# Kernel tuning notes

Hardware: AMD Instinct MI355X
Metric: run time of the kernel (lower is better)

Reference implementation:

```python
import jax, jax.numpy as jnp
import numpy as np

EPS = 1e-5

def _bn(z, g, b):
    # train-mode BatchNorm2d: batch stats over (B,H,W), biased variance
    mean = z.mean(axis=(0, 2, 3), keepdims=True)
    var = z.var(axis=(0, 2, 3), keepdims=True)
    return g[None, :, None, None] * (z - mean) * jax.lax.rsqrt(var + EPS) + b[None, :, None, None]

def _conv1x1(x, w):
    # x: [B,C,H,W], w: [O,C] -> [B,O,H,W]
    return jnp.einsum('bchw,oc->bohw', x, w)

def _proj(x, w1, g1, b1, w2, g2, b2):
    z = _bn(_conv1x1(x, w1), g1, b1)
    return _bn(_conv1x1(z, w2), g2, b2)

def setup_inputs() -> dict:
    key = jax.random.key(0)
    ks = jax.random.split(key, 24)
    B, Cx, Cy, M, H, W = 4, 512, 256, 64, 64, 64
    f32 = jnp.float32
    def wmat(k, o, c):
        return jax.random.normal(k, (o, c), f32) * (c ** -0.5)
    def gamma(k, c):
        return 1.0 + 0.1 * jax.random.normal(k, (c,), f32)
    def beta(k, c):
        return 0.1 * jax.random.normal(k, (c,), f32)
    inp = {
        'x': jax.random.normal(ks[0], (B, Cx, H, W), f32),
        'y': jax.random.normal(ks[1], (B, Cy, H, W), f32),
        # f_self
        'ws1': wmat(ks[2], M, Cx), 'gs1': gamma(ks[3], M), 'bs1': beta(ks[4], M),
        'ws2': wmat(ks[5], M, M),  'gs2': gamma(ks[6], M), 'bs2': beta(ks[7], M),
        # f_x
        'wx1': wmat(ks[8], M, Cx), 'gx1': gamma(ks[9], M), 'bx1': beta(ks[10], M),
        'wx2': wmat(ks[11], M, M), 'gx2': gamma(ks[12], M), 'bx2': beta(ks[13], M),
        # f_y
        'wy1': wmat(ks[14], M, Cy), 'gy1': gamma(ks[15], M), 'by1': beta(ks[16], M),
        'wy2': wmat(ks[17], M, M),  'gy2': gamma(ks[18], M), 'by2': beta(ks[19], M),
        # f_up
        'wu': wmat(ks[20], Cx, M), 'gu': gamma(ks[21], Cx), 'bu': beta(ks[22], Cx),
    }
    return inp

def reference(x, y, ws1, gs1, bs1, ws2, gs2, bs2,
              wx1, gx1, bx1, wx2, gx2, bx2,
              wy1, gy1, by1, wy2, gy2, by2,
              wu, gu, bu):
    B, C, H, W = x.shape
    M = ws1.shape[0]
    N = H * W
    fself = _proj(x, ws1, gs1, bs1, ws2, gs2, bs2).reshape(B, M, N).transpose(0, 2, 1)  # [B,N,M]
    fx = _proj(x, wx1, gx1, bx1, wx2, gx2, bx2).reshape(B, M, N).transpose(0, 2, 1)      # [B,N,M]
    fy = _proj(y, wy1, gy1, by1, wy2, gy2, by2).reshape(B, M, N)                          # [B,M,N]
    sim = jnp.matmul(fx, fy)                  # [B,N,N]  (scale=False)
    attn = jax.nn.softmax(sim, axis=-1)
    fout = jnp.matmul(attn, fself)            # [B,N,M]
    fout = fout.transpose(0, 2, 1).reshape(B, M, H, W)
    out = _bn(_conv1x1(fout, wu), gu, bu)
    return x + out
```

## Files before the change

### kernel.cpp

```cpp
#include <hip/hip_runtime.h>
#include <hip/hip_fp16.h>
#include <cstdint>

constexpr int N_ = 4096;
constexpr float CNT = 16384.f;

typedef __attribute__((ext_vector_type(8))) _Float16 half8;
typedef __attribute__((ext_vector_type(4))) float f32x4;
union fragh { half8 h8; int i4[4]; };

__device__ inline int pkh(float a, float b) {
  union { __half2 h; int i; } u;
  u.h = __float22half2_rn(float2{a, b});
  return u.i;
}


__global__ __launch_bounds__(256) void conv1_k(
    const float* __restrict__ x, const float* __restrict__ y,
    const float* __restrict__ ws1, const float* __restrict__ wx1,
    const float* __restrict__ wy1,
    float* __restrict__ z1s, float* __restrict__ z1x, float* __restrict__ z1y,
    float* __restrict__ stats) {
  const int t = threadIdx.x;
  const int slice = blockIdx.x;
  const int b = slice >> 5;
  const int n0 = (slice & 31) * 128;
  const int branch = blockIdx.y;
  const float* A = branch == 2 ? y : x;
  const float* W = branch == 0 ? ws1 : (branch == 1 ? wx1 : wy1);
  float* out = branch == 0 ? z1s : (branch == 1 ? z1x : z1y);
  const int K = branch == 2 ? 256 : 512;
  float* st = stats + branch * 128;

  __shared__ float sA[32][132];
  __shared__ float sW[32][72];

  const int to = (t >> 5) * 8;
  const int tn = (t & 31) * 4;
  float acc[8][4];
#pragma unroll
  for (int i = 0; i < 8; ++i)
#pragma unroll
    for (int j = 0; j < 4; ++j) acc[i][j] = 0.f;

  const float* Ab = A + (size_t)b * K * N_ + n0;
#pragma unroll 1
  for (int k0 = 0; k0 < K; k0 += 32) {
    __syncthreads();
#pragma unroll
    for (int i = 0; i < 4; ++i) {
      int row = i * 8 + (t >> 5);
      float4 v = *(const float4*)&Ab[(size_t)(k0 + row) * N_ + tn];
      *(float4*)&sA[row][tn] = v;
    }
    {
      int o = t >> 2, kk = (t & 3) * 8;
      float4 w0 = *(const float4*)&W[(size_t)o * K + k0 + kk];
      float4 w1 = *(const float4*)&W[(size_t)o * K + k0 + kk + 4];
      sW[kk + 0][o] = w0.x; sW[kk + 1][o] = w0.y;
      sW[kk + 2][o] = w0.z; sW[kk + 3][o] = w0.w;
      sW[kk + 4][o] = w1.x; sW[kk + 5][o] = w1.y;
      sW[kk + 6][o] = w1.z; sW[kk + 7][o] = w1.w;
    }
    __syncthreads();
#pragma unroll
    for (int k = 0; k < 32; ++k) {
      float4 a = *(const float4*)&sA[k][tn];
      float4 w0 = *(const float4*)&sW[k][to];
      float4 w1 = *(const float4*)&sW[k][to + 4];
      float wv[8] = {w0.x, w0.y, w0.z, w0.w, w1.x, w1.y, w1.z, w1.w};
      float av[4] = {a.x, a.y, a.z, a.w};
#pragma unroll
      for (int i = 0; i < 8; ++i)
#pragma unroll
        for (int j = 0; j < 4; ++j) acc[i][j] += wv[i] * av[j];
    }
  }
  float* Cb = out + (size_t)b * 64 * N_ + n0;
#pragma unroll
  for (int i = 0; i < 8; ++i) {
    float4 v = {acc[i][0], acc[i][1], acc[i][2], acc[i][3]};
    *(float4*)&Cb[(size_t)(to + i) * N_ + tn] = v;
  }
#pragma unroll
  for (int i = 0; i < 8; ++i) {
    float s = acc[i][0] + acc[i][1] + acc[i][2] + acc[i][3];
    float q = acc[i][0] * acc[i][0] + acc[i][1] * acc[i][1] +
              acc[i][2] * acc[i][2] + acc[i][3] * acc[i][3];
#pragma unroll
    for (int d = 1; d < 32; d <<= 1) { s += __shfl_xor(s, d); q += __shfl_xor(q, d); }
    if ((t & 31) == 0) { atomicAdd(&st[to + i], s); atomicAdd(&st[64 + to + i], q); }
  }
}

__global__ __launch_bounds__(256) void conv2_k(
    const float* __restrict__ z1s, const float* __restrict__ z1x,
    const float* __restrict__ z1y,
    const float* __restrict__ ws2, const float* __restrict__ wx2,
    const float* __restrict__ wy2,
    const float* __restrict__ gs1, const float* __restrict__ bs1,
    const float* __restrict__ gx1, const float* __restrict__ bx1,
    const float* __restrict__ gy1, const float* __restrict__ by1,
    float* __restrict__ z2s, float* __restrict__ z2x, float* __restrict__ z2y,
    float* __restrict__ stats) {
  const int t = threadIdx.x;
  const int slice = blockIdx.x;
  const int b = slice >> 5;
  const int n0 = (slice & 31) * 128;
  const int branch = blockIdx.y;
  const float* A = branch == 0 ? z1s : (branch == 1 ? z1x : z1y);
  const float* W = branch == 0 ? ws2 : (branch == 1 ? wx2 : wy2);
  const float* g1 = branch == 0 ? gs1 : (branch == 1 ? gx1 : gy1);
  const float* b1 = branch == 0 ? bs1 : (branch == 1 ? bx1 : by1);
  float* out = branch == 0 ? z2s : (branch == 1 ? z2x : z2y);
  const float* stin = stats + branch * 128;
  float* stout = stats + (3 + branch) * 128;

  __shared__ float sA[32][132];
  __shared__ float sW[32][72];
  __shared__ float sc[64], sh[64];

  if (t < 64) {
    float mean = stin[t] * (1.f / CNT);
    float var = stin[64 + t] * (1.f / CNT) - mean * mean;
    float r = rsqrtf(var + 1e-5f);
    float s = g1[t] * r;
    sc[t] = s;
    sh[t] = b1[t] - mean * s;
  }

  const int to = (t >> 5) * 8;
  const int tn = (t & 31) * 4;
  float acc[8][4];
#pragma unroll
  for (int i = 0; i < 8; ++i)
#pragma unroll
    for (int j = 0; j < 4; ++j) acc[i][j] = 0.f;

  const float* Ab = A + (size_t)b * 64 * N_ + n0;
#pragma unroll 1
  for (int k0 = 0; k0 < 64; k0 += 32) {
    __syncthreads();
#pragma unroll
    for (int i = 0; i < 4; ++i) {
      int row = i * 8 + (t >> 5);
      float4 v = *(const float4*)&Ab[(size_t)(k0 + row) * N_ + tn];
      float s = sc[k0 + row], h = sh[k0 + row];
      v.x = v.x * s + h; v.y = v.y * s + h; v.z = v.z * s + h; v.w = v.w * s + h;
      *(float4*)&sA[row][tn] = v;
    }
    {
      int o = t >> 2, kk = (t & 3) * 8;
      float4 w0 = *(const float4*)&W[(size_t)o * 64 + k0 + kk];
      float4 w1 = *(const float4*)&W[(size_t)o * 64 + k0 + kk + 4];
      sW[kk + 0][o] = w0.x; sW[kk + 1][o] = w0.y;
      sW[kk + 2][o] = w0.z; sW[kk + 3][o] = w0.w;
      sW[kk + 4][o] = w1.x; sW[kk + 5][o] = w1.y;
      sW[kk + 6][o] = w1.z; sW[kk + 7][o] = w1.w;
    }
    __syncthreads();
#pragma unroll
    for (int k = 0; k < 32; ++k) {
      float4 a = *(const float4*)&sA[k][tn];
      float4 w0 = *(const float4*)&sW[k][to];
      float4 w1 = *(const float4*)&sW[k][to + 4];
      float wv[8] = {w0.x, w0.y, w0.z, w0.w, w1.x, w1.y, w1.z, w1.w};
      float av[4] = {a.x, a.y, a.z, a.w};
#pragma unroll
      for (int i = 0; i < 8; ++i)
#pragma unroll
        for (int j = 0; j < 4; ++j) acc[i][j] += wv[i] * av[j];
    }
  }
  float* Cb = out + (size_t)b * 64 * N_ + n0;
#pragma unroll
  for (int i = 0; i < 8; ++i) {
    float4 v = {acc[i][0], acc[i][1], acc[i][2], acc[i][3]};
    *(float4*)&Cb[(size_t)(to + i) * N_ + tn] = v;
  }
#pragma unroll
  for (int i = 0; i < 8; ++i) {
    float s = acc[i][0] + acc[i][1] + acc[i][2] + acc[i][3];
    float q = acc[i][0] * acc[i][0] + acc[i][1] * acc[i][1] +
              acc[i][2] * acc[i][2] + acc[i][3] * acc[i][3];
#pragma unroll
    for (int d = 1; d < 32; d <<= 1) { s += __shfl_xor(s, d); q += __shfl_xor(q, d); }
    if ((t & 31) == 0) { atomicAdd(&stout[to + i], s); atomicAdd(&stout[64 + to + i], q); }
  }
}

__global__ __launch_bounds__(256) void pack_k(
    const float* __restrict__ z2s, const float* __restrict__ z2x,
    const float* __restrict__ z2y,
    const float* __restrict__ gs2, const float* __restrict__ bs2,
    const float* __restrict__ gx2, const float* __restrict__ bx2,
    const float* __restrict__ gy2, const float* __restrict__ by2,
    int* __restrict__ Qh, int* __restrict__ Kh, int* __restrict__ Vp,
    const float* __restrict__ stats) {
  const int job = blockIdx.z;
  const int idx = blockIdx.x * 256 + threadIdx.x;
  const float* z2 = job == 0 ? z2x : (job == 1 ? z2y : z2s);
  const float* g2 = job == 0 ? gx2 : (job == 1 ? gy2 : gs2);
  const float* b2 = job == 0 ? bx2 : (job == 1 ? by2 : bs2);
  const float* st = stats + (job == 0 ? 4 : (job == 1 ? 5 : 3)) * 128;
  int* outp = job == 0 ? Qh : (job == 1 ? Kh : Vp);

  auto snorm = [&](int c, float& s, float& h) {
    float mean = st[c] * (1.f / CNT);
    float var = st[64 + c] * (1.f / CNT) - mean * mean;
    float r = rsqrtf(var + 1e-5f);
    s = g2[c] * r;
    h = b2[c] - mean * s;
  };
  if (job < 2) {
    int n = idx & 4095, c = (idx >> 12) & 31, b = idx >> 17;
    float s0, h0, s1, h1;
    snorm(2 * c, s0, h0);
    snorm(2 * c + 1, s1, h1);
    float v0 = z2[((size_t)b * 64 + 2 * c) * N_ + n] * s0 + h0;
    float v1 = z2[((size_t)b * 64 + 2 * c + 1) * N_ + n] * s1 + h1;
    outp[idx] = pkh(v0, v1);
  } else {
    int k = idx & 2047, ch = (idx >> 11) & 63, b = idx >> 17;
    float s0, h0;
    snorm(ch, s0, h0);
    float2 v = *(const float2*)&z2[((size_t)b * 64 + ch) * N_ + 2 * k];
    outp[idx] = pkh(v.x * s0 + h0, v.y * s0 + h0);
  }
}

__global__ __launch_bounds__(256) void attn_k(const int* __restrict__ Qh,
                                              const int* __restrict__ Kh,
                                              const int* __restrict__ Vp,
                                              float* __restrict__ fout) {
  const int tid = threadIdx.x;
  const int lane = tid & 63;
  const int wid = tid >> 6;
  const int la = lane & 15;
  const int quad = lane >> 4;
  const int b = blockIdx.x & 3;
  const int qbase = (blockIdx.x >> 2) * 16;
  const int* Qb = Qh + (size_t)b * 32 * N_;
  const int* Kb = Kh + (size_t)b * 32 * N_;
  const int* Vb = Vp + (size_t)b * 64 * 2048;

  __shared__ union USm {
    float P[4][16 * 36];
    struct { float O[4][16][68]; float M[4][16]; float L[4][16]; } e;
  } smu;
  float* myP = smu.P[wid];

  fragh aq[2];
#pragma unroll
  for (int c = 0; c < 2; ++c)
#pragma unroll
    for (int j = 0; j < 4; ++j)
      aq[c].i4[j] = Qb[(size_t)(c * 16 + quad * 4 + j) * N_ + qbase + la];

  f32x4 o[4];
  float mrun[4], lrun[4];
#pragma unroll
  for (int mt = 0; mt < 4; ++mt) o[mt] = f32x4{0.f, 0.f, 0.f, 0.f};
#pragma unroll
  for (int r = 0; r < 4; ++r) { mrun[r] = -3.0e38f; lrun[r] = 0.f; }

  const int jbeg = wid * (N_ / 4);
#pragma unroll 1
  for (int j0 = jbeg; j0 < jbeg + N_ / 4; j0 += 32) {
    f32x4 s[2];
#pragma unroll
    for (int nt = 0; nt < 2; ++nt) {
      fragh k0, k1;
      const int key = j0 + nt * 16 + la;
#pragma unroll
      for (int jj = 0; jj < 4; ++jj) {
        k0.i4[jj] = Kb[(size_t)(quad * 4 + jj) * N_ + key];
        k1.i4[jj] = Kb[(size_t)(16 + quad * 4 + jj) * N_ + key];
      }
      f32x4 z = f32x4{0.f, 0.f, 0.f, 0.f};
      z = __builtin_amdgcn_mfma_f32_16x16x32_f16(aq[0].h8, k0.h8, z, 0, 0, 0);
      s[nt] = __builtin_amdgcn_mfma_f32_16x16x32_f16(aq[1].h8, k1.h8, z, 0, 0, 0);
    }
    float alpha[4];
#pragma unroll
    for (int r = 0; r < 4; ++r) {
      float t = fmaxf(s[0][r], s[1][r]);
      t = fmaxf(t, __shfl_xor(t, 1));
      t = fmaxf(t, __shfl_xor(t, 2));
      t = fmaxf(t, __shfl_xor(t, 4));
      t = fmaxf(t, __shfl_xor(t, 8));
      float mnew = fmaxf(mrun[r], t);
      alpha[r] = __expf(mrun[r] - mnew);
      float p0 = __expf(s[0][r] - mnew);
      float p1 = __expf(s[1][r] - mnew);
      s[0][r] = p0; s[1][r] = p1;
      float ps = p0 + p1;
      ps += __shfl_xor(ps, 1);
      ps += __shfl_xor(ps, 2);
      ps += __shfl_xor(ps, 4);
      ps += __shfl_xor(ps, 8);
      lrun[r] = lrun[r] * alpha[r] + ps;
      mrun[r] = mnew;
    }
#pragma unroll
    for (int nt = 0; nt < 2; ++nt)
#pragma unroll
      for (int r = 0; r < 4; ++r)
        myP[(quad * 4 + r) * 36 + nt * 16 + la] = s[nt][r];
    __asm__ __volatile__("s_waitcnt lgkmcnt(0)" ::: "memory");
    fragh pa;
    {
      const f32x4* pr = (const f32x4*)&myP[la * 36 + quad * 8];
      f32x4 p0 = pr[0], p1 = pr[1];
      pa.i4[0] = pkh(p0[0], p0[1]);
      pa.i4[1] = pkh(p0[2], p0[3]);
      pa.i4[2] = pkh(p1[0], p1[1]);
      pa.i4[3] = pkh(p1[2], p1[3]);
    }
#pragma unroll
    for (int mt = 0; mt < 4; ++mt)
#pragma unroll
      for (int r = 0; r < 4; ++r) o[mt][r] *= alpha[r];
#pragma unroll
    for (int mt = 0; mt < 4; ++mt) {
      const int4 vv = *(const int4*)&Vb[(size_t)(mt * 16 + la) * 2048 + (j0 >> 1) + quad * 4];
      fragh vb;
      vb.i4[0] = vv.x; vb.i4[1] = vv.y; vb.i4[2] = vv.z; vb.i4[3] = vv.w;
      o[mt] = __builtin_amdgcn_mfma_f32_16x16x32_f16(pa.h8, vb.h8, o[mt], 0, 0, 0);
    }
  }

  __syncthreads();
  if (la == 0) {
#pragma unroll
    for (int r = 0; r < 4; ++r) {
      smu.e.M[wid][quad * 4 + r] = mrun[r];
      smu.e.L[wid][quad * 4 + r] = lrun[r];
    }
  }
#pragma unroll
  for (int mt = 0; mt < 4; ++mt)
#pragma unroll
    for (int r = 0; r < 4; ++r) smu.e.O[wid][quad * 4 + r][mt * 16 + la] = o[mt][r];
  __syncthreads();

#pragma unroll
  for (int t = 0; t < 4; ++t) {
    int oidx = t * 256 + tid;
    int m = oidx >> 4;
    int q = oidx & 15;
    float m0 = fmaxf(fmaxf(smu.e.M[0][q], smu.e.M[1][q]),
                     fmaxf(smu.e.M[2][q], smu.e.M[3][q]));
    float num = 0.f, den = 0.f;
#pragma unroll
    for (int w = 0; w < 4; ++w) {
      float wgt = __expf(smu.e.M[w][q] - m0);
      num += wgt * smu.e.O[w][q][m];
      den += wgt * smu.e.L[w][q];
    }
    fout[((size_t)b * 64 + m) * N_ + qbase + q] = num / den;
  }
}

__global__ __launch_bounds__(256) void convup_k(const float* __restrict__ fout,
                                                const float* __restrict__ wu,
                                                float* __restrict__ u,
                                                float* __restrict__ stats) {
  const int t = threadIdx.x;
  const int slice = blockIdx.x;
  const int b = slice >> 5;
  const int n0 = (slice & 31) * 128;
  const int o0 = blockIdx.y * 64;

  __shared__ float sA[32][132];
  __shared__ float sW[32][72];

  const int to = (t >> 5) * 8;
  const int tn = (t & 31) * 4;
  float acc[8][4];
#pragma unroll
  for (int i = 0; i < 8; ++i)
#pragma unroll
    for (int j = 0; j < 4; ++j) acc[i][j] = 0.f;

  const float* Ab = fout + (size_t)b * 64 * N_ + n0;
#pragma unroll 1
  for (int k0 = 0; k0 < 64; k0 += 32) {
    __syncthreads();
#pragma unroll
    for (int i = 0; i < 4; ++i) {
      int row = i * 8 + (t >> 5);
      float4 v = *(const float4*)&Ab[(size_t)(k0 + row) * N_ + tn];
      *(float4*)&sA[row][tn] = v;
    }
    {
      int o = t >> 2, kk = (t & 3) * 8;
      float4 w0 = *(const float4*)&wu[(size_t)(o0 + o) * 64 + k0 + kk];
      float4 w1 = *(const float4*)&wu[(size_t)(o0 + o) * 64 + k0 + kk + 4];
      sW[kk + 0][o] = w0.x; sW[kk + 1][o] = w0.y;
      sW[kk + 2][o] = w0.z; sW[kk + 3][o] = w0.w;
      sW[kk + 4][o] = w1.x; sW[kk + 5][o] = w1.y;
      sW[kk + 6][o] = w1.z; sW[kk + 7][o] = w1.w;
    }
    __syncthreads();
#pragma unroll
    for (int k = 0; k < 32; ++k) {
      float4 a = *(const float4*)&sA[k][tn];
      float4 w0 = *(const float4*)&sW[k][to];
      float4 w1 = *(const float4*)&sW[k][to + 4];
      float wv[8] = {w0.x, w0.y, w0.z, w0.w, w1.x, w1.y, w1.z, w1.w};
      float av[4] = {a.x, a.y, a.z, a.w};
#pragma unroll
      for (int i = 0; i < 8; ++i)
#pragma unroll
        for (int j = 0; j < 4; ++j) acc[i][j] += wv[i] * av[j];
    }
  }
  float* Cb = u + ((size_t)b * 512 + o0) * N_ + n0;
#pragma unroll
  for (int i = 0; i < 8; ++i) {
    float4 v = {acc[i][0], acc[i][1], acc[i][2], acc[i][3]};
    *(float4*)&Cb[(size_t)(to + i) * N_ + tn] = v;
  }
#pragma unroll
  for (int i = 0; i < 8; ++i) {
    float s = acc[i][0] + acc[i][1] + acc[i][2] + acc[i][3];
    float q = acc[i][0] * acc[i][0] + acc[i][1] * acc[i][1] +
              acc[i][2] * acc[i][2] + acc[i][3] * acc[i][3];
#pragma unroll
    for (int d = 1; d < 32; d <<= 1) { s += __shfl_xor(s, d); q += __shfl_xor(q, d); }
    if ((t & 31) == 0) {
      atomicAdd(&stats[768 + o0 + to + i], s);
      atomicAdd(&stats[1280 + o0 + to + i], q);
    }
  }
}

__global__ __launch_bounds__(256) void final_k(const float* __restrict__ x,
                                               const float* __restrict__ u,
                                               const float* __restrict__ gu,
                                               const float* __restrict__ bu,
                                               const float* __restrict__ stats,
                                               float* __restrict__ out) {
  size_t idx = (size_t)blockIdx.x * 256 + threadIdx.x;
  int c = (int)((idx >> 12) & 511);
  float mean = stats[768 + c] * (1.f / CNT);
  float var = stats[1280 + c] * (1.f / CNT) - mean * mean;
  float r = rsqrtf(var + 1e-5f);
  float s = gu[c] * r;
  float sh = bu[c] - mean * s;
  out[idx] = x[idx] + u[idx] * s + sh;
}

extern "C" void kernel_launch(void* const* d_in, const int* in_sizes, int n_in,
                              void* d_out, int out_size, void* d_ws, size_t ws_size,
                              hipStream_t stream) {
  const float* x = (const float*)d_in[0];
  const float* y = (const float*)d_in[1];
  const float* ws1 = (const float*)d_in[2];
  const float* gs1 = (const float*)d_in[3];
  const float* bs1 = (const float*)d_in[4];
  const float* ws2 = (const float*)d_in[5];
  const float* gs2 = (const float*)d_in[6];
  const float* bs2 = (const float*)d_in[7];
  const float* wx1 = (const float*)d_in[8];
  const float* gx1 = (const float*)d_in[9];
  const float* bx1 = (const float*)d_in[10];
  const float* wx2 = (const float*)d_in[11];
  const float* gx2 = (const float*)d_in[12];
  const float* bx2 = (const float*)d_in[13];
  const float* wy1 = (const float*)d_in[14];
  const float* gy1 = (const float*)d_in[15];
  const float* by1 = (const float*)d_in[16];
  const float* wy2 = (const float*)d_in[17];
  const float* gy2 = (const float*)d_in[18];
  const float* by2 = (const float*)d_in[19];
  const float* wu = (const float*)d_in[20];
  const float* gu = (const float*)d_in[21];
  const float* bu = (const float*)d_in[22];
  float* out = (float*)d_out;

  float* w = (float*)d_ws;
  const size_t M1 = 1048576;
  float* z1s = w + 0 * M1;
  float* z1x = w + 1 * M1;
  float* z1y = w + 2 * M1;
  float* z2s = w + 3 * M1;
  float* z2x = w + 4 * M1;
  float* z2y = w + 5 * M1;
  float* fout = w + 6 * M1;
  float* u = w + 7 * M1;
  int* Qh = (int*)(w + 15 * M1);
  int* Kh = Qh + 524288;
  int* Vp = Kh + 524288;
  float* stats = (float*)(Vp + 524288);

  hipMemsetAsync(stats, 0, 1792 * sizeof(float), stream);

  conv1_k<<<dim3(128, 3), dim3(256), 0, stream>>>(x, y, ws1, wx1, wy1, z1s, z1x,
                                                  z1y, stats);
  conv2_k<<<dim3(128, 3), dim3(256), 0, stream>>>(
      z1s, z1x, z1y, ws2, wx2, wy2, gs1, bs1, gx1, bx1, gy1, by1, z2s, z2x, z2y,
      stats);
  pack_k<<<dim3(2048, 1, 3), dim3(256), 0, stream>>>(z2s, z2x, z2y, gs2, bs2, gx2,
                                                     bx2, gy2, by2, Qh, Kh, Vp,
                                                     stats);
  attn_k<<<dim3(1024), dim3(256), 0, stream>>>(Qh, Kh, Vp, fout);
  convup_k<<<dim3(128, 8), dim3(256), 0, stream>>>(fout, wu, u, stats);
  final_k<<<dim3(32768), dim3(256), 0, stream>>>(x, u, gu, bu, stats, out);
}
```

Before: 407.2 us.

## Restructure attention to transposed MFMA with key-major K, tiled V, exp2 softmax

Splits the pack kernel into three per-tensor kernels. K is now stored key-major (via an LDS transpose) and V in 32-key tiles, so the attention loop loads K and V fragments with contiguous int4 reads instead of strided scalar loads. The attention MFMAs are swapped so S^T is computed, which leaves each lane owning one query column. This removes the per-row shuffle reductions and the LDS round-trip for P, and the P fragment is packed directly from registers. log2(e) is folded into Q's normalization so the softmax can use exp2f, and launch bounds now request 4 blocks per CU. The cost is two extra kernel launches and more fragile fragment-layout bookkeeping.

Result: slower. 427.5 us (+5.0%).

```diff
diff --git a/kernel.cpp b/kernel.cpp
--- a/kernel.cpp
+++ b/kernel.cpp
@@ -4,10 +4,11 @@
 
 constexpr int N_ = 4096;
 constexpr float CNT = 16384.f;
+constexpr float LOG2E = 1.4426950408889634f;
 
 typedef __attribute__((ext_vector_type(8))) _Float16 half8;
 typedef __attribute__((ext_vector_type(4))) float f32x4;
-union fragh { half8 h8; int i4[4]; };
+union fragh { half8 h8; int i4[4]; int4 v4; };
 
 __device__ inline int pkh(float a, float b) {
   union { __half2 h; int i; } u;
@@ -190,50 +191,92 @@
   }
 }
 
-__global__ __launch_bounds__(256) void pack_k(
-    const float* __restrict__ z2s, const float* __restrict__ z2x,
-    const float* __restrict__ z2y,
-    const float* __restrict__ gs2, const float* __restrict__ bs2,
-    const float* __restrict__ gx2, const float* __restrict__ bx2,
-    const float* __restrict__ gy2, const float* __restrict__ by2,
-    int* __restrict__ Qh, int* __restrict__ Kh, int* __restrict__ Vp,
-    const float* __restrict__ stats) {
-  const int job = blockIdx.z;
+__global__ __launch_bounds__(256) void packQ_k(const float* __restrict__ z2x,
+                                               const float* __restrict__ gx2,
+                                               const float* __restrict__ bx2,
+                                               int* __restrict__ Qh,
+                                               const float* __restrict__ stats) {
   const int idx = blockIdx.x * 256 + threadIdx.x;
-  const float* z2 = job == 0 ? z2x : (job == 1 ? z2y : z2s);
-  const float* g2 = job == 0 ? gx2 : (job == 1 ? gy2 : gs2);
-  const float* b2 = job == 0 ? bx2 : (job == 1 ? by2 : bs2);
-  const float* st = stats + (job == 0 ? 4 : (job == 1 ? 5 : 3)) * 128;
-  int* outp = job == 0 ? Qh : (job == 1 ? Kh : Vp);
-
-  auto snorm = [&](int c, float& s, float& h) {
-    float mean = st[c] * (1.f / CNT);
-    float var = st[64 + c] * (1.f / CNT) - mean * mean;
+  const float* st = stats + 4 * 128;
+  int n = idx & 4095, c = (idx >> 12) & 31, b = idx >> 17;
+  auto snorm = [&](int ch, float& s, float& h) {
+    float mean = st[ch] * (1.f / CNT);
+    float var = st[64 + ch] * (1.f / CNT) - mean * mean;
     float r = rsqrtf(var + 1e-5f);
-    s = g2[c] * r;
-    h = b2[c] - mean * s;
+    s = gx2[ch] * r * LOG2E;
+    h = (bx2[ch] - mean * gx2[ch] * r) * LOG2E;
   };
-  if (job < 2) {
-    int n = idx & 4095, c = (idx >> 12) & 31, b = idx >> 17;
-    float s0, h0, s1, h1;
-    snorm(2 * c, s0, h0);
-    snorm(2 * c + 1, s1, h1);
-    float v0 = z2[((size_t)b * 64 + 2 * c) * N_ + n] * s0 + h0;
-    float v1 = z2[((size_t)b * 64 + 2 * c + 1) * N_ + n] * s1 + h1;
-    outp[idx] = pkh(v0, v1);
-  } else {
-    int k = idx & 2047, ch = (idx >> 11) & 63, b = idx >> 17;
-    float s0, h0;
-    snorm(ch, s0, h0);
-    float2 v = *(const float2*)&z2[((size_t)b * 64 + ch) * N_ + 2 * k];
-    outp[idx] = pkh(v.x * s0 + h0, v.y * s0 + h0);
-  }
-}
-
-__global__ __launch_bounds__(256) void attn_k(const int* __restrict__ Qh,
-                                              const int* __restrict__ Kh,
-                                              const int* __restrict__ Vp,
-                                              float* __restrict__ fout) {
+  float s0, h0, s1, h1;
+  snorm(2 * c, s0, h0);
+  snorm(2 * c + 1, s1, h1);
+  float v0 = z2x[((size_t)b * 64 + 2 * c) * N_ + n] * s0 + h0;
+  float v1 = z2x[((size_t)b * 64 + 2 * c + 1) * N_ + n] * s1 + h1;
+  Qh[idx] = pkh(v0, v1);
+}
+
+__global__ __launch_bounds__(256) void packK_k(const float* __restrict__ z2y,
+                                               const float* __restrict__ gy2,
+                                               const float* __restrict__ by2,
+                                               int* __restrict__ Kh,
+                                               const float* __restrict__ stats) {
+  const int t = threadIdx.x;
+  const int key0 = blockIdx.x * 64;
+  const int b = blockIdx.y;
+  const float* st = stats + 5 * 128;
+  __shared__ float tile[64][68];
+  __shared__ float sc[64], sh[64];
+  if (t < 64) {
+    float mean = st[t] * (1.f / CNT);
+    float var = st[64 + t] * (1.f / CNT) - mean * mean;
+    float r = rsqrtf(var + 1e-5f);
+    float s = gy2[t] * r;
+    sc[t] = s;
+    sh[t] = by2[t] - mean * s;
+  }
+  __syncthreads();
+#pragma unroll
+  for (int it = 0; it < 4; ++it) {
+    int lin = it * 256 + t;
+    int ch = lin >> 4, f4i = lin & 15;
+    float4 v = *(const float4*)&z2y[((size_t)b * 64 + ch) * N_ + key0 + f4i * 4];
+    float s = sc[ch], h = sh[ch];
+    v.x = v.x * s + h; v.y = v.y * s + h; v.z = v.z * s + h; v.w = v.w * s + h;
+    *(float4*)&tile[ch][f4i * 4] = v;
+  }
+  __syncthreads();
+  const int key = t >> 2, cg = t & 3;
+  int outv[8];
+#pragma unroll
+  for (int i = 0; i < 8; ++i) {
+    int c = cg * 8 + i;
+    outv[i] = pkh(tile[2 * c][key], tile[2 * c + 1][key]);
+  }
+  int* dst = Kh + ((size_t)b * N_ + key0 + key) * 32 + cg * 8;
+  *(int4*)dst = *(int4*)&outv[0];
+  *(int4*)(dst + 4) = *(int4*)&outv[4];
+}
+
+__global__ __launch_bounds__(256) void packV_k(const float* __restrict__ z2s,
+                                               const float* __restrict__ gs2,
+                                               const float* __restrict__ bs2,
+                                               int* __restrict__ Vp,
+                                               const float* __restrict__ stats) {
+  const int idx = blockIdx.x * 256 + threadIdx.x;
+  const float* st = stats + 3 * 128;
+  int pil = idx & 15, ch = (idx >> 4) & 63, pb = (idx >> 10) & 127, b = idx >> 17;
+  float mean = st[ch] * (1.f / CNT);
+  float var = st[64 + ch] * (1.f / CNT) - mean * mean;
+  float r = rsqrtf(var + 1e-5f);
+  float s = gs2[ch] * r;
+  float h = bs2[ch] - mean * s;
+  float2 v = *(const float2*)&z2s[((size_t)b * 64 + ch) * N_ + pb * 32 + pil * 2];
+  Vp[idx] = pkh(v.x * s + h, v.y * s + h);
+}
+
+__global__ __launch_bounds__(256, 4) void attn_k(const int* __restrict__ Qh,
+                                                 const int* __restrict__ Kh,
+                                                 const int* __restrict__ Vp,
+                                                 float* __restrict__ fout) {
   const int tid = threadIdx.x;
   const int lane = tid & 63;
   const int wid = tid >> 6;
@@ -243,106 +286,90 @@
   const int qbase = (blockIdx.x >> 2) * 16;
   const int* Qb = Qh + (size_t)b * 32 * N_;
   const int* Kb = Kh + (size_t)b * 32 * N_;
-  const int* Vb = Vp + (size_t)b * 64 * 2048;
-
-  __shared__ union USm {
-    float P[4][16 * 36];
-    struct { float O[4][16][68]; float M[4][16]; float L[4][16]; } e;
-  } smu;
-  float* myP = smu.P[wid];
-
-  fragh aq[2];
-#pragma unroll
-  for (int c = 0; c < 2; ++c)
-#pragma unroll
-    for (int j = 0; j < 4; ++j)
-      aq[c].i4[j] = Qb[(size_t)(c * 16 + quad * 4 + j) * N_ + qbase + la];
+  const int* Vb = Vp + (size_t)b * 128 * 1024;
+
+  __shared__ struct { float O[4][16][68]; float M[4][16]; float L[4][16]; } sm;
+
+  fragh qb[2];
+#pragma unroll
+  for (int h = 0; h < 2; ++h)
+#pragma unroll
+    for (int jj = 0; jj < 4; ++jj)
+      qb[h].i4[jj] = Qb[(size_t)(h * 16 + quad * 4 + jj) * N_ + qbase + la];
+
+  const int keyrow = (la & 3) + ((la >> 2) << 3);
 
   f32x4 o[4];
-  float mrun[4], lrun[4];
 #pragma unroll
   for (int mt = 0; mt < 4; ++mt) o[mt] = f32x4{0.f, 0.f, 0.f, 0.f};
-#pragma unroll
-  for (int r = 0; r < 4; ++r) { mrun[r] = -3.0e38f; lrun[r] = 0.f; }
-
-  const int jbeg = wid * (N_ / 4);
+  float mrun = -3.0e38f, lrun = 0.f;
+
+  const int jbeg = wid * 1024;
+  const int* kptr = Kb + (jbeg + keyrow) * 32 + quad * 4;
+  const int* vptr = Vb + (jbeg >> 5) * 1024 + la * 16 + quad * 4;
 #pragma unroll 1
-  for (int j0 = jbeg; j0 < jbeg + N_ / 4; j0 += 32) {
+  for (int it = 0; it < 32; ++it) {
+    fragh ka[2][2];
+#pragma unroll
+    for (int nt = 0; nt < 2; ++nt)
+#pragma unroll
+      for (int h = 0; h < 2; ++h)
+        ka[nt][h].v4 = *(const int4*)(kptr + nt * 128 + h * 16);
+    fragh va[4];
+#pragma unroll
+    for (int mt = 0; mt < 4; ++mt) va[mt].v4 = *(const int4*)(vptr + mt * 256);
+    kptr += 1024;
+    vptr += 1024;
     f32x4 s[2];
 #pragma unroll
     for (int nt = 0; nt < 2; ++nt) {
-      fragh k0, k1;
-      const int key = j0 + nt * 16 + la;
-#pragma unroll
-      for (int jj = 0; jj < 4; ++jj) {
-        k0.i4[jj] = Kb[(size_t)(quad * 4 + jj) * N_ + key];
-        k1.i4[jj] = Kb[(size_t)(16 + quad * 4 + jj) * N_ + key];
+      f32x4 z = f32x4{0.f, 0.f, 0.f, 0.f};
+      z = __builtin_amdgcn_mfma_f32_16x16x32_f16(ka[nt][0].h8, qb[0].h8, z, 0, 0, 0);
+      s[nt] = __builtin_amdgcn_mfma_f32_16x16x32_f16(ka[nt][1].h8, qb[1].h8, z, 0, 0, 0);
+    }
+    float t0 = fmaxf(fmaxf(s[0][0], s[0][1]), fmaxf(s[0][2], s[0][3]));
+    float t1 = fmaxf(fmaxf(s[1][0], s[1][1]), fmaxf(s[1][2], s[1][3]));
+    float t = fmaxf(t0, t1);
+    t = fmaxf(t, __shfl_xor(t, 16));
+    t = fmaxf(t, __shfl_xor(t, 32));
+    float mnew = fmaxf(mrun, t);
+    float alpha = exp2f(mrun - mnew);
+    float p[2][4];
+    float ps = 0.f;
+#pragma unroll
+    for (int nt = 0; nt < 2; ++nt)
+#pragma unroll
+      for (int r = 0; r < 4; ++r) {
+        p[nt][r] = exp2f(s[nt][r] - mnew);
+        ps += p[nt][r];
       }
-      f32x4 z = f32x4{0.f, 0.f, 0.f, 0.f};
-      z = __builtin_amdgcn_mfma_f32_16x16x32_f16(aq[0].h8, k0.h8, z, 0, 0, 0);
-      s[nt] = __builtin_amdgcn_mfma_f32_16x16x32_f16(aq[1].h8, k1.h8, z, 0, 0, 0);
-    }
-    float alpha[4];
-#pragma unroll
-    for (int r = 0; r < 4; ++r) {
-      float t = fmaxf(s[0][r], s[1][r]);
-      t = fmaxf(t, __shfl_xor(t, 1));
-      t = fmaxf(t, __shfl_xor(t, 2));
-      t = fmaxf(t, __shfl_xor(t, 4));
-      t = fmaxf(t, __shfl_xor(t, 8));
-      float mnew = fmaxf(mrun[r], t);
-      alpha[r] = __expf(mrun[r] - mnew);
-      float p0 = __expf(s[0][r] - mnew);
-      float p1 = __expf(s[1][r] - mnew);
-      s[0][r] = p0; s[1][r] = p1;
-      float ps = p0 + p1;
-      ps += __shfl_xor(ps, 1);
-      ps += __shfl_xor(ps, 2);
-      ps += __shfl_xor(ps, 4);
-      ps += __shfl_xor(ps, 8);
-      lrun[r] = lrun[r] * alpha[r] + ps;
-      mrun[r] = mnew;
-    }
-#pragma unroll
-    for (int nt = 0; nt < 2; ++nt)
-#pragma unroll
-      for (int r = 0; r < 4; ++r)
-        myP[(quad * 4 + r) * 36 + nt * 16 + la] = s[nt][r];
-    __asm__ __volatile__("s_waitcnt lgkmcnt(0)" ::: "memory");
-    fragh pa;
-    {
-      const f32x4* pr = (const f32x4*)&myP[la * 36 + quad * 8];
-      f32x4 p0 = pr[0], p1 = pr[1];
-      pa.i4[0] = pkh(p0[0], p0[1]);
-      pa.i4[1] = pkh(p0[2], p0[3]);
-      pa.i4[2] = pkh(p1[0], p1[1]);
-      pa.i4[3] = pkh(p1[2], p1[3]);
-    }
-#pragma unroll
-    for (int mt = 0; mt < 4; ++mt)
-#pragma unroll
-      for (int r = 0; r < 4; ++r) o[mt][r] *= alpha[r];
+    lrun = lrun * alpha + ps;
+    mrun = mnew;
+    fragh pf;
+    pf.i4[0] = pkh(p[0][0], p[0][1]);
+    pf.i4[1] = pkh(p[0][2], p[0][3]);
+    pf.i4[2] = pkh(p[1][0], p[1][1]);
+    pf.i4[3] = pkh(p[1][2], p[1][3]);
 #pragma unroll
     for (int mt = 0; mt < 4; ++mt) {
-      const int4 vv = *(const int4*)&Vb[(size_t)(mt * 16 + la) * 2048 + (j0 >> 1) + quad * 4];
-      fragh vb;
-      vb.i4[0] = vv.x; vb.i4[1] = vv.y; vb.i4[2] = vv.z; vb.i4[3] = vv.w;
-      o[mt] = __builtin_amdgcn_mfma_f32_16x16x32_f16(pa.h8, vb.h8, o[mt], 0, 0, 0);
-    }
-  }
-
-  __syncthreads();
-  if (la == 0) {
-#pragma unroll
-    for (int r = 0; r < 4; ++r) {
-      smu.e.M[wid][quad * 4 + r] = mrun[r];
-      smu.e.L[wid][quad * 4 + r] = lrun[r];
-    }
+#pragma unroll
+      for (int r = 0; r < 4; ++r) o[mt][r] *= alpha;
+      o[mt] = __builtin_amdgcn_mfma_f32_16x16x32_f16(va[mt].h8, pf.h8, o[mt], 0, 0, 0);
+    }
+  }
+
+  float lw = lrun;
+  lw += __shfl_xor(lw, 16);
+  lw += __shfl_xor(lw, 32);
+  if (lane < 16) {
+    sm.M[wid][la] = mrun;
+    sm.L[wid][la] = lw;
   }
 #pragma unroll
   for (int mt = 0; mt < 4; ++mt)
 #pragma unroll
-    for (int r = 0; r < 4; ++r) smu.e.O[wid][quad * 4 + r][mt * 16 + la] = o[mt][r];
+    for (int r = 0; r < 4; ++r)
+      sm.O[wid][la][mt * 16 + quad * 4 + r] = o[mt][r];
   __syncthreads();
 
 #pragma unroll
@@ -350,14 +377,13 @@
     int oidx = t * 256 + tid;
     int m = oidx >> 4;
     int q = oidx & 15;
-    float m0 = fmaxf(fmaxf(smu.e.M[0][q], smu.e.M[1][q]),
-                     fmaxf(smu.e.M[2][q], smu.e.M[3][q]));
+    float m0 = fmaxf(fmaxf(sm.M[0][q], sm.M[1][q]), fmaxf(sm.M[2][q], sm.M[3][q]));
     float num = 0.f, den = 0.f;
 #pragma unroll
     for (int w = 0; w < 4; ++w) {
-      float wgt = __expf(smu.e.M[w][q] - m0);
-      num += wgt * smu.e.O[w][q][m];
-      den += wgt * smu.e.L[w][q];
+      float wgt = exp2f(sm.M[w][q] - m0);
+      num += wgt * sm.O[w][q][m];
+      den += wgt * sm.L[w][q];
     }
     fout[((size_t)b * 64 + m) * N_ + qbase + q] = num / den;
   }
@@ -503,9 +529,9 @@
   conv2_k<<<dim3(128, 3), dim3(256), 0, stream>>>(
       z1s, z1x, z1y, ws2, wx2, wy2, gs1, bs1, gx1, bx1, gy1, by1, z2s, z2x, z2y,
       stats);
-  pack_k<<<dim3(2048, 1, 3), dim3(256), 0, stream>>>(z2s, z2x, z2y, gs2, bs2, gx2,
-                                                     bx2, gy2, by2, Qh, Kh, Vp,
-                                                     stats);
+  packQ_k<<<dim3(2048), dim3(256), 0, stream>>>(z2x, gx2, bx2, Qh, stats);
+  packK_k<<<dim3(64, 4), dim3(256), 0, stream>>>(z2y, gy2, by2, Kh, stats);
+  packV_k<<<dim3(2048), dim3(256), 0, stream>>>(z2s, gs2, bs2, Vp, stats);
   attn_k<<<dim3(1024), dim3(256), 0, stream>>>(Qh, Kh, Vp, fout);
   convup_k<<<dim3(128, 8), dim3(256), 0, stream>>>(fout, wu, u, stats);
   final_k<<<dim3(32768), dim3(256), 0, stream>>>(x, u, gu, bu, stats, out);
```
